# Optimization experiments

Measured on AMD Instinct MI355X. Metric: run time of the kernel, lower is better.

The kernel has to match this reference:

```python
import jax, jax.numpy as jnp
import numpy as np

B, N, C_IN, C_OUT, M = 32, 4096, 128, 128, 256


def setup_inputs() -> dict:
    key = jax.random.key(0)
    k1, k2, k3, k4 = jax.random.split(key, 4)
    x = jax.random.normal(k1, (B, N, C_IN), dtype=jnp.float32)
    # Lowest-M eigenvectors of a graph Laplacian are orthonormal columns [N, M];
    # build an equivalent orthonormal basis via QR of a random matrix.
    U, _ = jnp.linalg.qr(jax.random.normal(k2, (N, M), dtype=jnp.float32))
    # complex spectral weights ~ 0.02 * randn (cfloat) split into real/imag parts
    W_real = jax.random.normal(k3, (C_IN, C_OUT, M), dtype=jnp.float32) * 0.02
    W_imag = jax.random.normal(k4, (C_IN, C_OUT, M), dtype=jnp.float32) * 0.02
    return {"x": x, "eigenvectors": U, "W_real": W_real, "W_imag": W_imag}


def reference(x, eigenvectors, W_real, W_imag):
    # Graph Fourier transform: project node features onto spectral modes.
    # x_spec[b, m, c] = sum_n U[n, m] * x[b, n, c]
    x_spec = jnp.einsum('nm,bnc->bmc', eigenvectors, x)  # [B, M, C_in], real
    # Per-mode complex channel mixing, fused into one batched einsum.
    # Original takes .real of (x_spec * W); since x_spec is real,
    # Re(x_spec @ W) = x_spec @ Re(W), so W_imag does not affect the output.
    out_spec_real = jnp.einsum('bmc,com->bmo', x_spec, W_real)  # [B, M, C_out]
    # Inverse graph Fourier transform back to node space.
    return jnp.einsum('nm,bmo->bno', eigenvectors, out_spec_real)  # [B, N, C_out]
```

## Files before the change

kernel.cpp:

```cpp
#include <hip/hip_runtime.h>
#include <hip/hip_bf16.h>

#define BB 32
#define NN 4096
#define CI 128
#define CO 128
#define MM 256
#define KS 8

typedef __hip_bfloat16 bf16;
typedef __attribute__((ext_vector_type(8))) short bf16x8;
typedef __attribute__((ext_vector_type(4))) float f32x4;

__device__ inline void gl_lds16(const void* g, void* l) {
    __builtin_amdgcn_global_load_lds(
        (const __attribute__((address_space(1))) void*)g,
        (__attribute__((address_space(3))) void*)l, 16, 0, 0);
}

__global__ __launch_bounds__(256) void k_cvtU(const float* __restrict__ U,
                                              bf16* __restrict__ Un,
                                              bf16* __restrict__ Ut) {
    const int n0 = blockIdx.x * 64;
    const int m0 = blockIdx.y * 64;
    __shared__ float tile[64][65];
    const int t = threadIdx.x;
    #pragma unroll
    for (int i = 0; i < 16; ++i) {
        int lin = t + i * 256;
        int r = lin >> 6, c = lin & 63;
        float v = U[(n0 + r) * MM + m0 + c];
        tile[r][c] = v;
        Un[(n0 + r) * MM + m0 + c] = __float2bfloat16(v);
    }
    __syncthreads();
    #pragma unroll
    for (int pass = 0; pass < 2; ++pass) {
        int no = t & 7;
        int m  = (t >> 3) + pass * 32;
        bf16 tmp[8];
        #pragma unroll
        for (int j = 0; j < 8; ++j) tmp[j] = __float2bfloat16(tile[no * 8 + j][m]);
        *(bf16x8*)&Ut[(long)(m0 + m) * NN + n0 + no * 8] = *(bf16x8*)tmp;
    }
}

__global__ __launch_bounds__(256) void k_wt(const float* __restrict__ W,
                                            bf16* __restrict__ Wt) {
    const int m0 = blockIdx.x * 64;
    const int o0 = blockIdx.y * 64;
    const int c  = blockIdx.z;
    __shared__ float tile[64][65];
    const int t = threadIdx.x;
    #pragma unroll
    for (int pass = 0; pass < 4; ++pass) {
        int r  = (t >> 4) + pass * 16;
        int m4 = (t & 15) * 4;
        float4 v = *(const float4*)&W[((long)c * CO + o0 + r) * MM + m0 + m4];
        tile[r][m4 + 0] = v.x; tile[r][m4 + 1] = v.y;
        tile[r][m4 + 2] = v.z; tile[r][m4 + 3] = v.w;
    }
    __syncthreads();
    #pragma unroll
    for (int pass = 0; pass < 2; ++pass) {
        int oo = t & 7;
        int m  = (t >> 3) + pass * 32;
        bf16 tmp[8];
        #pragma unroll
        for (int j = 0; j < 8; ++j) tmp[j] = __float2bfloat16(tile[oo * 8 + j][m]);
        *(bf16x8*)&Wt[((long)(m0 + m) * CI + c) * CO + o0 + oo * 8] = *(bf16x8*)tmp;
    }
}

__global__ __launch_bounds__(512) void k_gemm1f(const bf16* __restrict__ Ut,
                                                const float* __restrict__ x,
                                                bf16* __restrict__ part) {
    const int ks = blockIdx.x;
    const int b  = blockIdx.y;
    __shared__ __align__(16) bf16  As[2][MM * 32];
    __shared__ __align__(16) bf16  Bs[2][CI * 32];
    __shared__ __align__(16) float Xf[2][32 * CI];
    const int t    = threadIdx.x;
    const int lane = t & 63;
    const int wave = t >> 6;
    const int wm   = wave >> 1, wn = wave & 1;
    const int fr   = lane & 15;
    const int kg   = (lane >> 4) * 8;
    f32x4 acc[4][4] = {};
    const long xrow  = (long)b * NN;
    const int  kbase = ks * 512;

    auto STAGE = [&](int buf, int kt) {
        const int k0 = kbase + kt * 32;
        #pragma unroll
        for (int i = 0; i < 2; ++i) {
            int lin = t + i * 512;
            {
                int r = lin >> 2, kk = (lin & 3) * 8;
                gl_lds16(&Ut[(long)r * NN + k0 + kk], &As[buf][lin * 8]);
            }
            {
                int r = lin >> 5, c4 = (lin & 31) * 4;
                gl_lds16(&x[(xrow + k0 + r) * CI + c4], &Xf[buf][lin * 4]);
            }
        }
    };

    const int NT = 512 / 32;
    STAGE(0, 0);
    __syncthreads();
    #pragma unroll
    for (int kt = 0; kt < NT; ++kt) {
        const int cur = kt & 1;
        if (kt + 1 < NT) STAGE(cur ^ 1, kt + 1);
        {
            const int c  = t & 127;
            const int nh = t >> 7;
            bf16 tmp[8];
            #pragma unroll
            for (int j = 0; j < 8; ++j)
                tmp[j] = __float2bfloat16(Xf[cur][(nh * 8 + j) * CI + c]);
            *(bf16x8*)&Bs[cur][c * 32 + nh * 8] = *(bf16x8*)tmp;
        }
        __syncthreads();
        bf16x8 a[4], bfr[4];
        #pragma unroll
        for (int i = 0; i < 4; ++i)
            a[i] = *(const bf16x8*)&As[cur][(wm * 64 + i * 16 + fr) * 32 + kg];
        #pragma unroll
        for (int j = 0; j < 4; ++j)
            bfr[j] = *(const bf16x8*)&Bs[cur][(wn * 64 + j * 16 + fr) * 32 + kg];
        #pragma unroll
        for (int i = 0; i < 4; ++i)
            #pragma unroll
            for (int j = 0; j < 4; ++j)
                acc[i][j] = __builtin_amdgcn_mfma_f32_16x16x32_bf16(a[i], bfr[j], acc[i][j], 0, 0, 0);
        __syncthreads();
    }
    const int quad = (lane >> 4) * 4;
    const long pbase = ((long)ks * BB + b) * MM * CI;
    #pragma unroll
    for (int i = 0; i < 4; ++i) {
        #pragma unroll
        for (int j = 0; j < 4; ++j) {
            int mg = wm * 64 + i * 16 + quad;
            int cg = wn * 64 + j * 16 + fr;
            #pragma unroll
            for (int r = 0; r < 4; ++r)
                part[pbase + (long)(mg + r) * CI + cg] = __float2bfloat16(acc[i][j][r]);
        }
    }
}

__global__ __launch_bounds__(256) void k_mix(const bf16* __restrict__ part,
                                             const bf16* __restrict__ Wt,
                                             bf16* __restrict__ osT) {
    const int blk = blockIdx.x;
    const int m   = (blk & 7) * 32 + (blk >> 3);
    __shared__ bf16  Wl[CI][CO];
    __shared__ float xl[CI][36];
    const int t = threadIdx.x;
    const long wb = (long)m * CI * CO;
    #pragma unroll
    for (int i = 0; i < 8; ++i) {
        int ch = t + i * 256;
        int c = ch >> 4, og = (ch & 15) * 8;
        *(bf16x8*)&Wl[c][og] = *(const bf16x8*)&Wt[wb + (long)c * CO + og];
    }
    #pragma unroll
    for (int i = 0; i < 2; ++i) {
        int ch = t + i * 256;
        int b = ch >> 4, c8 = (ch & 15) * 8;
        float s[8] = {};
        #pragma unroll
        for (int ks = 0; ks < KS; ++ks) {
            bf16x8 v = *(const bf16x8*)&part[(((long)ks * BB + b) * MM + m) * CI + c8];
            #pragma unroll
            for (int j = 0; j < 8; ++j) s[j] += __bfloat162float(((const bf16*)&v)[j]);
        }
        #pragma unroll
        for (int j = 0; j < 8; ++j) xl[c8 + j][b] = s[j];
    }
    __syncthreads();
    const int o  = t & 127;
    const int bh = t >> 7;
    float acc[16] = {};
    for (int c = 0; c < CI; ++c) {
        float w = __bfloat162float(Wl[c][o]);
        #pragma unroll
        for (int j = 0; j < 16; ++j)
            acc[j] += xl[c][bh * 16 + j] * w;
    }
    #pragma unroll
    for (int j = 0; j < 16; ++j)
        osT[((long)(bh * 16 + j) * CO + o) * MM + m] = __float2bfloat16(acc[j]);
}

__global__ __launch_bounds__(256) void k_gemm3(const bf16* __restrict__ Un,
                                               const bf16* __restrict__ osT,
                                               float* __restrict__ out) {
    const int n0 = blockIdx.x * 128;
    const int b  = blockIdx.y;
    __shared__ __align__(16) bf16 As[128 * 32];
    __shared__ __align__(16) bf16 Bs[128 * 32];
    const int t    = threadIdx.x;
    const int lane = t & 63;
    const int wave = t >> 6;
    const int wm   = wave >> 1, wn = wave & 1;
    const int fr   = lane & 15;
    const int kg   = (lane >> 4) * 8;
    f32x4 acc[4][4] = {};
    const long bbase = (long)b * CO * MM;
    for (int kt = 0; kt < MM / 32; ++kt) {
        const int k0 = kt * 32;
        #pragma unroll
        for (int i = 0; i < 2; ++i) {
            int lin = t + i * 256;
            int r = lin >> 2, kk = (lin & 3) * 8;
            gl_lds16(&Un[(long)(n0 + r) * MM + k0 + kk], &As[lin * 8]);
            gl_lds16(&osT[bbase + (long)r * MM + k0 + kk], &Bs[lin * 8]);
        }
        __syncthreads();
        bf16x8 a[4], bfr[4];
        #pragma unroll
        for (int i = 0; i < 4; ++i)
            a[i] = *(const bf16x8*)&As[(wm * 64 + i * 16 + fr) * 32 + kg];
        #pragma unroll
        for (int j = 0; j < 4; ++j)
            bfr[j] = *(const bf16x8*)&Bs[(wn * 64 + j * 16 + fr) * 32 + kg];
        #pragma unroll
        for (int i = 0; i < 4; ++i)
            #pragma unroll
            for (int j = 0; j < 4; ++j)
                acc[i][j] = __builtin_amdgcn_mfma_f32_16x16x32_bf16(a[i], bfr[j], acc[i][j], 0, 0, 0);
        __syncthreads();
    }
    const int quad = (lane >> 4) * 4;
    #pragma unroll
    for (int i = 0; i < 4; ++i) {
        #pragma unroll
        for (int j = 0; j < 4; ++j) {
            int ng = n0 + wm * 64 + i * 16 + quad;
            int og = wn * 64 + j * 16 + fr;
            #pragma unroll
            for (int r = 0; r < 4; ++r)
                out[((long)b * NN + ng + r) * CO + og] = acc[i][j][r];
        }
    }
}

extern "C" void kernel_launch(void* const* d_in, const int* in_sizes, int n_in,
                              void* d_out, int out_size, void* d_ws, size_t ws_size,
                              hipStream_t stream) {
    const float* x  = (const float*)d_in[0];
    const float* U  = (const float*)d_in[1];
    const float* Wr = (const float*)d_in[2];
    float* out = (float*)d_out;

    char* p = (char*)d_ws;
    bf16* part = (bf16*)p;  p += (size_t)KS * BB * MM * CI * 2;
    bf16* Ut   = (bf16*)p;  p += (size_t)MM * NN * 2;
    bf16* Un   = (bf16*)p;  p += (size_t)NN * MM * 2;
    bf16* osT  = (bf16*)p;  p += (size_t)BB * CO * MM * 2;
    bf16* Wt   = (bf16*)p;  p += (size_t)MM * CI * CO * 2;

    k_cvtU  <<<dim3(NN / 64, MM / 64), 256, 0, stream>>>(U, Un, Ut);
    k_wt    <<<dim3(MM / 64, CO / 64, CI), 256, 0, stream>>>(Wr, Wt);
    k_gemm1f<<<dim3(KS, BB), 512, 0, stream>>>(Ut, x, part);
    k_mix   <<<dim3(256), 256, 0, stream>>>(part, Wt, osT);
    k_gemm3 <<<dim3(NN / 128, BB), 256, 0, stream>>>(Un, osT, out);
}
```

Baseline: 187.7 us.

## Double-buffer gemm3 LDS loads with explicit vmcnt waits and reorder gemm1 prefetch

```diff
diff --git a/kernel.cpp b/kernel.cpp
--- a/kernel.cpp
+++ b/kernel.cpp
@@ -17,6 +17,9 @@
         (const __attribute__((address_space(1))) void*)g,
         (__attribute__((address_space(3))) void*)l, 16, 0, 0);
 }
+
+#define CFENCE() asm volatile("" ::: "memory")
+#define BAR()    __builtin_amdgcn_s_barrier()
 
 __global__ __launch_bounds__(256) void k_cvtU(const float* __restrict__ U,
                                               bf16* __restrict__ Un,
@@ -112,7 +115,6 @@
     #pragma unroll
     for (int kt = 0; kt < NT; ++kt) {
         const int cur = kt & 1;
-        if (kt + 1 < NT) STAGE(cur ^ 1, kt + 1);
         {
             const int c  = t & 127;
             const int nh = t >> 7;
@@ -123,6 +125,7 @@
             *(bf16x8*)&Bs[cur][c * 32 + nh * 8] = *(bf16x8*)tmp;
         }
         __syncthreads();
+        if (kt + 1 < NT) STAGE(cur ^ 1, kt + 1);
         bf16x8 a[4], bfr[4];
         #pragma unroll
         for (int i = 0; i < 4; ++i)
@@ -201,8 +204,8 @@
                                                float* __restrict__ out) {
     const int n0 = blockIdx.x * 128;
     const int b  = blockIdx.y;
-    __shared__ __align__(16) bf16 As[128 * 32];
-    __shared__ __align__(16) bf16 Bs[128 * 32];
+    __shared__ __align__(16) bf16 As[2][128 * 32];
+    __shared__ __align__(16) bf16 Bs[2][128 * 32];
     const int t    = threadIdx.x;
     const int lane = t & 63;
     const int wave = t >> 6;
@@ -211,29 +214,43 @@
     const int kg   = (lane >> 4) * 8;
     f32x4 acc[4][4] = {};
     const long bbase = (long)b * CO * MM;
-    for (int kt = 0; kt < MM / 32; ++kt) {
+
+    auto STAGE = [&](int buf, int kt) {
         const int k0 = kt * 32;
         #pragma unroll
         for (int i = 0; i < 2; ++i) {
             int lin = t + i * 256;
             int r = lin >> 2, kk = (lin & 3) * 8;
-            gl_lds16(&Un[(long)(n0 + r) * MM + k0 + kk], &As[lin * 8]);
-            gl_lds16(&osT[bbase + (long)r * MM + k0 + kk], &Bs[lin * 8]);
-        }
-        __syncthreads();
+            gl_lds16(&Un[(long)(n0 + r) * MM + k0 + kk], &As[buf][lin * 8]);
+            gl_lds16(&osT[bbase + (long)r * MM + k0 + kk], &Bs[buf][lin * 8]);
+        }
+    };
+
+    const int NT = MM / 32;
+    STAGE(0, 0);
+    #pragma unroll
+    for (int kt = 0; kt < NT; ++kt) {
+        const int cur = kt & 1;
+        if (kt + 1 < NT) {
+            STAGE(cur ^ 1, kt + 1);
+            asm volatile("s_waitcnt vmcnt(4)" ::: "memory");
+        } else {
+            asm volatile("s_waitcnt vmcnt(0)" ::: "memory");
+        }
+        BAR(); CFENCE();
         bf16x8 a[4], bfr[4];
         #pragma unroll
         for (int i = 0; i < 4; ++i)
-            a[i] = *(const bf16x8*)&As[(wm * 64 + i * 16 + fr) * 32 + kg];
+            a[i] = *(const bf16x8*)&As[cur][(wm * 64 + i * 16 + fr) * 32 + kg];
         #pragma unroll
         for (int j = 0; j < 4; ++j)
-            bfr[j] = *(const bf16x8*)&Bs[(wn * 64 + j * 16 + fr) * 32 + kg];
+            bfr[j] = *(const bf16x8*)&Bs[cur][(wn * 64 + j * 16 + fr) * 32 + kg];
         #pragma unroll
         for (int i = 0; i < 4; ++i)
             #pragma unroll
             for (int j = 0; j < 4; ++j)
                 acc[i][j] = __builtin_amdgcn_mfma_f32_16x16x32_bf16(a[i], bfr[j], acc[i][j], 0, 0, 0);
-        __syncthreads();
+        CFENCE(); BAR(); CFENCE();
     }
     const int quad = (lane >> 4) * 4;
     #pragma unroll
```

After: 187.5 us. Within noise of the previous version (-0.1%).

## Fuse all five stages into one cooperative persistent kernel with grid syncs

Applied to the files above, without the earlier changes.

```diff
diff --git a/kernel.cpp b/kernel.cpp
--- a/kernel.cpp
+++ b/kernel.cpp
@@ -1,5 +1,8 @@
 #include <hip/hip_runtime.h>
 #include <hip/hip_bf16.h>
+#include <hip/hip_cooperative_groups.h>
+
+namespace cg = cooperative_groups;
 
 #define BB 32
 #define NN 4096
@@ -16,6 +19,251 @@
     __builtin_amdgcn_global_load_lds(
         (const __attribute__((address_space(1))) void*)g,
         (__attribute__((address_space(3))) void*)l, 16, 0, 0);
+}
+
+__global__ __launch_bounds__(256, 2) void k_all(const float* __restrict__ x,
+                                                const float* __restrict__ U,
+                                                const float* __restrict__ W,
+                                                float* __restrict__ out,
+                                                bf16* __restrict__ part,
+                                                bf16* __restrict__ Ut,
+                                                bf16* __restrict__ Un,
+                                                bf16* __restrict__ osT,
+                                                bf16* __restrict__ Wt) {
+    cg::grid_group grid = cg::this_grid();
+    const int blk = blockIdx.x;
+    const int t   = threadIdx.x;
+    __shared__ __align__(16) char smem[64 * 1024];
+
+    if (blk < 256) {
+        const int n0 = (blk & 63) * 64;
+        const int m0 = (blk >> 6) * 64;
+        float (*tile)[65] = (float(*)[65])smem;
+        #pragma unroll
+        for (int i = 0; i < 16; ++i) {
+            int lin = t + i * 256;
+            int r = lin >> 6, c = lin & 63;
+            float v = U[(n0 + r) * MM + m0 + c];
+            tile[r][c] = v;
+            Un[(n0 + r) * MM + m0 + c] = __float2bfloat16(v);
+        }
+        __syncthreads();
+        #pragma unroll
+        for (int pass = 0; pass < 2; ++pass) {
+            int no = t & 7;
+            int m  = (t >> 3) + pass * 32;
+            bf16 tmp[8];
+            #pragma unroll
+            for (int j = 0; j < 8; ++j) tmp[j] = __float2bfloat16(tile[no * 8 + j][m]);
+            *(bf16x8*)&Ut[(long)(m0 + m) * NN + n0 + no * 8] = *(bf16x8*)tmp;
+        }
+    } else {
+        const int q  = blk - 256;
+        const int m0 = (q & 3) * 64;
+        const int o0 = ((q >> 2) & 1) * 64;
+        const int cb = q >> 3;
+        float (*tile)[65] = (float(*)[65])smem;
+        for (int ci = 0; ci < 4; ++ci) {
+            const int c = cb * 4 + ci;
+            #pragma unroll
+            for (int pass = 0; pass < 4; ++pass) {
+                int r  = (t >> 4) + pass * 16;
+                int m4 = (t & 15) * 4;
+                float4 v = *(const float4*)&W[((long)c * CO + o0 + r) * MM + m0 + m4];
+                tile[r][m4 + 0] = v.x; tile[r][m4 + 1] = v.y;
+                tile[r][m4 + 2] = v.z; tile[r][m4 + 3] = v.w;
+            }
+            __syncthreads();
+            #pragma unroll
+            for (int pass = 0; pass < 2; ++pass) {
+                int oo = t & 7;
+                int m  = (t >> 3) + pass * 32;
+                bf16 tmp[8];
+                #pragma unroll
+                for (int j = 0; j < 8; ++j) tmp[j] = __float2bfloat16(tile[oo * 8 + j][m]);
+                *(bf16x8*)&Wt[((long)(m0 + m) * CI + c) * CO + o0 + oo * 8] = *(bf16x8*)tmp;
+            }
+            __syncthreads();
+        }
+    }
+    __threadfence();
+    grid.sync();
+
+    {
+        const int ks = blk & 7;
+        const int mt = (blk >> 3) & 1;
+        const int b  = blk >> 4;
+        const int m0 = mt * 128;
+        bf16*  As = (bf16*)smem;
+        bf16*  Bs = (bf16*)(smem + 16 * 1024);
+        float* Xf = (float*)(smem + 32 * 1024);
+        const int lane = t & 63, wave = t >> 6;
+        const int wm = wave >> 1, wn = wave & 1;
+        const int fr = lane & 15, kg = (lane >> 4) * 8;
+        f32x4 acc[4][4] = {};
+        const long xrow  = (long)b * NN;
+        const int  kbase = ks * 512;
+
+        auto STAGE1 = [&](int buf, int kt) {
+            const int k0 = kbase + kt * 32;
+            #pragma unroll
+            for (int i = 0; i < 2; ++i) {
+                int lin = t + i * 256;
+                int r = lin >> 2, kk = (lin & 3) * 8;
+                gl_lds16(&Ut[(long)(m0 + r) * NN + k0 + kk], &As[buf * 4096 + lin * 8]);
+            }
+            #pragma unroll
+            for (int i = 0; i < 4; ++i) {
+                int lin = t + i * 256;
+                int r = lin >> 5, c4 = (lin & 31) * 4;
+                gl_lds16(&x[(xrow + k0 + r) * CI + c4], &Xf[buf * 4096 + lin * 4]);
+            }
+        };
+
+        STAGE1(0, 0);
+        __syncthreads();
+        for (int kt = 0; kt < 16; ++kt) {
+            const int cur = kt & 1;
+            {
+                const int c = t & 127;
+                #pragma unroll
+                for (int pass = 0; pass < 2; ++pass) {
+                    int no = (t >> 7) + pass * 2;
+                    bf16 tmp[8];
+                    #pragma unroll
+                    for (int j = 0; j < 8; ++j)
+                        tmp[j] = __float2bfloat16(Xf[cur * 4096 + (no * 8 + j) * CI + c]);
+                    *(bf16x8*)&Bs[cur * 4096 + c * 32 + no * 8] = *(bf16x8*)tmp;
+                }
+            }
+            __syncthreads();
+            if (kt + 1 < 16) STAGE1(cur ^ 1, kt + 1);
+            bf16x8 a[4], bfr[4];
+            #pragma unroll
+            for (int i = 0; i < 4; ++i)
+                a[i] = *(const bf16x8*)&As[cur * 4096 + (wm * 64 + i * 16 + fr) * 32 + kg];
+            #pragma unroll
+            for (int j = 0; j < 4; ++j)
+                bfr[j] = *(const bf16x8*)&Bs[cur * 4096 + (wn * 64 + j * 16 + fr) * 32 + kg];
+            #pragma unroll
+            for (int i = 0; i < 4; ++i)
+                #pragma unroll
+                for (int j = 0; j < 4; ++j)
+                    acc[i][j] = __builtin_amdgcn_mfma_f32_16x16x32_bf16(a[i], bfr[j], acc[i][j], 0, 0, 0);
+            __syncthreads();
+        }
+        const int quad = (lane >> 4) * 4;
+        const long pbase = ((long)ks * BB + b) * MM * CI;
+        #pragma unroll
+        for (int i = 0; i < 4; ++i) {
+            #pragma unroll
+            for (int j = 0; j < 4; ++j) {
+                int mg = m0 + wm * 64 + i * 16 + quad;
+                int cg = wn * 64 + j * 16 + fr;
+                #pragma unroll
+                for (int r = 0; r < 4; ++r)
+                    part[pbase + (long)(mg + r) * CI + cg] = __float2bfloat16(acc[i][j][r]);
+            }
+        }
+    }
+    __threadfence();
+    grid.sync();
+
+    {
+        const int mi = blk >> 1;
+        const int m  = (mi & 7) * 32 + (mi >> 3);
+        const int o0 = (blk & 1) * 64;
+        float* Wl = (float*)smem;
+        float* xl = (float*)(smem + 32 * 1024);
+        const long wb = (long)m * CI * CO;
+        #pragma unroll
+        for (int i = 0; i < 4; ++i) {
+            int ch = t + i * 256;
+            int c = ch >> 3, og = (ch & 7) * 8;
+            bf16x8 v = *(const bf16x8*)&Wt[wb + (long)c * CO + o0 + og];
+            #pragma unroll
+            for (int j = 0; j < 8; ++j) Wl[c * 64 + og + j] = __bfloat162float(((const bf16*)&v)[j]);
+        }
+        #pragma unroll
+        for (int i = 0; i < 2; ++i) {
+            int ch = t + i * 256;
+            int b2 = ch >> 4, c8 = (ch & 15) * 8;
+            float s[8] = {};
+            #pragma unroll
+            for (int ks = 0; ks < KS; ++ks) {
+                bf16x8 v = *(const bf16x8*)&part[(((long)ks * BB + b2) * MM + m) * CI + c8];
+                #pragma unroll
+                for (int j = 0; j < 8; ++j) s[j] += __bfloat162float(((const bf16*)&v)[j]);
+            }
+            #pragma unroll
+            for (int j = 0; j < 8; ++j) xl[(c8 + j) * 36 + b2] = s[j];
+        }
+        __syncthreads();
+        const int op = t & 63;
+        const int bq = t >> 6;
+        float acc[8] = {};
+        for (int c = 0; c < CI; ++c) {
+            float w = Wl[c * 64 + op];
+            #pragma unroll
+            for (int j = 0; j < 8; ++j)
+                acc[j] += xl[c * 36 + bq * 8 + j] * w;
+        }
+        #pragma unroll
+        for (int j = 0; j < 8; ++j)
+            osT[((long)(bq * 8 + j) * CO + o0 + op) * MM + m] = __float2bfloat16(acc[j]);
+    }
+    __threadfence();
+    grid.sync();
+
+    {
+        const int b3 = blk >> 4;
+        bf16* As3 = (bf16*)smem;
+        bf16* Bs3 = (bf16*)(smem + 8 * 1024);
+        const int lane = t & 63, wave = t >> 6;
+        const int wm = wave >> 1, wn = wave & 1;
+        const int fr = lane & 15, kg = (lane >> 4) * 8;
+        const long bbase = (long)b3 * CO * MM;
+        for (int rr = 0; rr < 2; ++rr) {
+            const int n0 = ((blk & 15) * 2 + rr) * 128;
+            f32x4 acc[4][4] = {};
+            for (int kt = 0; kt < MM / 32; ++kt) {
+                const int k0 = kt * 32;
+                #pragma unroll
+                for (int i = 0; i < 2; ++i) {
+                    int lin = t + i * 256;
+                    int r = lin >> 2, kk = (lin & 3) * 8;
+                    gl_lds16(&Un[(long)(n0 + r) * MM + k0 + kk], &As3[lin * 8]);
+                    gl_lds16(&osT[bbase + (long)r * MM + k0 + kk], &Bs3[lin * 8]);
+                }
+                __syncthreads();
+                bf16x8 a[4], bfr[4];
+                #pragma unroll
+                for (int i = 0; i < 4; ++i)
+                    a[i] = *(const bf16x8*)&As3[(wm * 64 + i * 16 + fr) * 32 + kg];
+                #pragma unroll
+                for (int j = 0; j < 4; ++j)
+                    bfr[j] = *(const bf16x8*)&Bs3[(wn * 64 + j * 16 + fr) * 32 + kg];
+                #pragma unroll
+                for (int i = 0; i < 4; ++i)
+                    #pragma unroll
+                    for (int j = 0; j < 4; ++j)
+                        acc[i][j] = __builtin_amdgcn_mfma_f32_16x16x32_bf16(a[i], bfr[j], acc[i][j], 0, 0, 0);
+                __syncthreads();
+            }
+            const int quad = (lane >> 4) * 4;
+            #pragma unroll
+            for (int i = 0; i < 4; ++i) {
+                #pragma unroll
+                for (int j = 0; j < 4; ++j) {
+                    int ng = n0 + wm * 64 + i * 16 + quad;
+                    int og = wn * 64 + j * 16 + fr;
+                    #pragma unroll
+                    for (int r = 0; r < 4; ++r)
+                        out[((long)b3 * NN + ng + r) * CO + og] = acc[i][j][r];
+                }
+            }
+        }
+    }
 }
 
 __global__ __launch_bounds__(256) void k_cvtU(const float* __restrict__ U,
@@ -112,7 +360,6 @@
     #pragma unroll
     for (int kt = 0; kt < NT; ++kt) {
         const int cur = kt & 1;
-        if (kt + 1 < NT) STAGE(cur ^ 1, kt + 1);
         {
             const int c  = t & 127;
             const int nh = t >> 7;
@@ -123,6 +370,7 @@
             *(bf16x8*)&Bs[cur][c * 32 + nh * 8] = *(bf16x8*)tmp;
         }
         __syncthreads();
+        if (kt + 1 < NT) STAGE(cur ^ 1, kt + 1);
         bf16x8 a[4], bfr[4];
         #pragma unroll
         for (int i = 0; i < 4; ++i)
@@ -264,9 +512,19 @@
     bf16* osT  = (bf16*)p;  p += (size_t)BB * CO * MM * 2;
     bf16* Wt   = (bf16*)p;  p += (size_t)MM * CI * CO * 2;
 
-    k_cvtU  <<<dim3(NN / 64, MM / 64), 256, 0, stream>>>(U, Un, Ut);
-    k_wt    <<<dim3(MM / 64, CO / 64, CI), 256, 0, stream>>>(Wr, Wt);
-    k_gemm1f<<<dim3(KS, BB), 512, 0, stream>>>(Ut, x, part);
-    k_mix   <<<dim3(256), 256, 0, stream>>>(part, Wt, osT);
-    k_gemm3 <<<dim3(NN / 128, BB), 256, 0, stream>>>(Un, osT, out);
-}
+    const float* xa = x; const float* Ua = U; const float* Wa = Wr;
+    float* outa = out;
+    bf16 *parta = part, *Uta = Ut, *Una = Un, *osTa = osT, *Wta = Wt;
+    void* args[] = {&xa, &Ua, &Wa, &outa, &parta, &Uta, &Una, &osTa, &Wta};
+
+    hipError_t err = hipLaunchCooperativeKernel((const void*)k_all,
+                                                dim3(512), dim3(256),
+                                                args, 0, stream);
+    if (err != hipSuccess) {
+        k_cvtU  <<<dim3(NN / 64, MM / 64), 256, 0, stream>>>(U, Un, Ut);
+        k_wt    <<<dim3(MM / 64, CO / 64, CI), 256, 0, stream>>>(Wr, Wt);
+        k_gemm1f<<<dim3(KS, BB), 512, 0, stream>>>(Ut, x, part);
+        k_mix   <<<dim3(256), 256, 0, stream>>>(part, Wt, osT);
+        k_gemm3 <<<dim3(NN / 128, BB), 256, 0, stream>>>(Un, osT, out);
+    }
+}
```

Result: slower. 579.0 us (+208.4%).

## Merge prep kernels into one launch and split GEMM1 into 128-row M tiles

Applied to the files above, without the earlier changes.

```diff
diff --git a/kernel.cpp b/kernel.cpp
--- a/kernel.cpp
+++ b/kernel.cpp
@@ -18,68 +18,72 @@
         (__attribute__((address_space(3))) void*)l, 16, 0, 0);
 }
 
-__global__ __launch_bounds__(256) void k_cvtU(const float* __restrict__ U,
+__global__ __launch_bounds__(256) void k_prep(const float* __restrict__ U,
+                                              const float* __restrict__ W,
                                               bf16* __restrict__ Un,
-                                              bf16* __restrict__ Ut) {
-    const int n0 = blockIdx.x * 64;
-    const int m0 = blockIdx.y * 64;
+                                              bf16* __restrict__ Ut,
+                                              bf16* __restrict__ Wt) {
+    const int blk = blockIdx.x;
+    const int t = threadIdx.x;
     __shared__ float tile[64][65];
-    const int t = threadIdx.x;
-    #pragma unroll
-    for (int i = 0; i < 16; ++i) {
-        int lin = t + i * 256;
-        int r = lin >> 6, c = lin & 63;
-        float v = U[(n0 + r) * MM + m0 + c];
-        tile[r][c] = v;
-        Un[(n0 + r) * MM + m0 + c] = __float2bfloat16(v);
-    }
-    __syncthreads();
-    #pragma unroll
-    for (int pass = 0; pass < 2; ++pass) {
-        int no = t & 7;
-        int m  = (t >> 3) + pass * 32;
-        bf16 tmp[8];
-        #pragma unroll
-        for (int j = 0; j < 8; ++j) tmp[j] = __float2bfloat16(tile[no * 8 + j][m]);
-        *(bf16x8*)&Ut[(long)(m0 + m) * NN + n0 + no * 8] = *(bf16x8*)tmp;
-    }
-}
-
-__global__ __launch_bounds__(256) void k_wt(const float* __restrict__ W,
-                                            bf16* __restrict__ Wt) {
-    const int m0 = blockIdx.x * 64;
-    const int o0 = blockIdx.y * 64;
-    const int c  = blockIdx.z;
-    __shared__ float tile[64][65];
-    const int t = threadIdx.x;
-    #pragma unroll
-    for (int pass = 0; pass < 4; ++pass) {
-        int r  = (t >> 4) + pass * 16;
-        int m4 = (t & 15) * 4;
-        float4 v = *(const float4*)&W[((long)c * CO + o0 + r) * MM + m0 + m4];
-        tile[r][m4 + 0] = v.x; tile[r][m4 + 1] = v.y;
-        tile[r][m4 + 2] = v.z; tile[r][m4 + 3] = v.w;
-    }
-    __syncthreads();
-    #pragma unroll
-    for (int pass = 0; pass < 2; ++pass) {
-        int oo = t & 7;
-        int m  = (t >> 3) + pass * 32;
-        bf16 tmp[8];
-        #pragma unroll
-        for (int j = 0; j < 8; ++j) tmp[j] = __float2bfloat16(tile[oo * 8 + j][m]);
-        *(bf16x8*)&Wt[((long)(m0 + m) * CI + c) * CO + o0 + oo * 8] = *(bf16x8*)tmp;
-    }
-}
-
-__global__ __launch_bounds__(512) void k_gemm1f(const bf16* __restrict__ Ut,
+    if (blk < 256) {
+        const int n0 = (blk & 63) * 64;
+        const int m0 = (blk >> 6) * 64;
+        #pragma unroll
+        for (int i = 0; i < 16; ++i) {
+            int lin = t + i * 256;
+            int r = lin >> 6, c = lin & 63;
+            float v = U[(n0 + r) * MM + m0 + c];
+            tile[r][c] = v;
+            Un[(n0 + r) * MM + m0 + c] = __float2bfloat16(v);
+        }
+        __syncthreads();
+        #pragma unroll
+        for (int pass = 0; pass < 2; ++pass) {
+            int no = t & 7;
+            int m  = (t >> 3) + pass * 32;
+            bf16 tmp[8];
+            #pragma unroll
+            for (int j = 0; j < 8; ++j) tmp[j] = __float2bfloat16(tile[no * 8 + j][m]);
+            *(bf16x8*)&Ut[(long)(m0 + m) * NN + n0 + no * 8] = *(bf16x8*)tmp;
+        }
+    } else {
+        const int q  = blk - 256;
+        const int c  = q >> 3;
+        const int m0 = (q & 3) * 64;
+        const int o0 = ((q >> 2) & 1) * 64;
+        #pragma unroll
+        for (int pass = 0; pass < 4; ++pass) {
+            int r  = (t >> 4) + pass * 16;
+            int m4 = (t & 15) * 4;
+            float4 v = *(const float4*)&W[((long)c * CO + o0 + r) * MM + m0 + m4];
+            tile[r][m4 + 0] = v.x; tile[r][m4 + 1] = v.y;
+            tile[r][m4 + 2] = v.z; tile[r][m4 + 3] = v.w;
+        }
+        __syncthreads();
+        #pragma unroll
+        for (int pass = 0; pass < 2; ++pass) {
+            int oo = t & 7;
+            int m  = (t >> 3) + pass * 32;
+            bf16 tmp[8];
+            #pragma unroll
+            for (int j = 0; j < 8; ++j) tmp[j] = __float2bfloat16(tile[oo * 8 + j][m]);
+            *(bf16x8*)&Wt[((long)(m0 + m) * CI + c) * CO + o0 + oo * 8] = *(bf16x8*)tmp;
+        }
+    }
+}
+
+__global__ __launch_bounds__(256) void k_gemm1f(const bf16* __restrict__ Ut,
                                                 const float* __restrict__ x,
                                                 bf16* __restrict__ part) {
-    const int ks = blockIdx.x;
-    const int b  = blockIdx.y;
-    __shared__ __align__(16) bf16  As[2][MM * 32];
-    __shared__ __align__(16) bf16  Bs[2][CI * 32];
-    __shared__ __align__(16) float Xf[2][32 * CI];
+    const int bx = blockIdx.x;
+    const int ks = bx & 7;
+    const int mt = (bx >> 3) & 1;
+    const int b  = bx >> 4;
+    const int m0 = mt * 128;
+    __shared__ __align__(16) bf16  As[2][128 * 32];
+    __shared__ __align__(16) bf16  Bs[2][128 * 32];
+    __shared__ __align__(16) float Xf[2][32 * 128];
     const int t    = threadIdx.x;
     const int lane = t & 63;
     const int wave = t >> 6;
@@ -94,35 +98,36 @@
         const int k0 = kbase + kt * 32;
         #pragma unroll
         for (int i = 0; i < 2; ++i) {
-            int lin = t + i * 512;
-            {
-                int r = lin >> 2, kk = (lin & 3) * 8;
-                gl_lds16(&Ut[(long)r * NN + k0 + kk], &As[buf][lin * 8]);
-            }
-            {
-                int r = lin >> 5, c4 = (lin & 31) * 4;
-                gl_lds16(&x[(xrow + k0 + r) * CI + c4], &Xf[buf][lin * 4]);
-            }
+            int lin = t + i * 256;
+            int r = lin >> 2, kk = (lin & 3) * 8;
+            gl_lds16(&Ut[(long)(m0 + r) * NN + k0 + kk], &As[buf][lin * 8]);
+        }
+        #pragma unroll
+        for (int i = 0; i < 4; ++i) {
+            int lin = t + i * 256;
+            int r = lin >> 5, c4 = (lin & 31) * 4;
+            gl_lds16(&x[(xrow + k0 + r) * CI + c4], &Xf[buf][lin * 4]);
         }
     };
 
-    const int NT = 512 / 32;
     STAGE(0, 0);
     __syncthreads();
-    #pragma unroll
-    for (int kt = 0; kt < NT; ++kt) {
+    for (int kt = 0; kt < 16; ++kt) {
         const int cur = kt & 1;
-        if (kt + 1 < NT) STAGE(cur ^ 1, kt + 1);
         {
-            const int c  = t & 127;
-            const int nh = t >> 7;
-            bf16 tmp[8];
-            #pragma unroll
-            for (int j = 0; j < 8; ++j)
-                tmp[j] = __float2bfloat16(Xf[cur][(nh * 8 + j) * CI + c]);
-            *(bf16x8*)&Bs[cur][c * 32 + nh * 8] = *(bf16x8*)tmp;
-        }
-        __syncthreads();
+            const int c = t & 127;
+            #pragma unroll
+            for (int pass = 0; pass < 2; ++pass) {
+                int no = (t >> 7) + pass * 2;
+                bf16 tmp[8];
+                #pragma unroll
+                for (int j = 0; j < 8; ++j)
+                    tmp[j] = __float2bfloat16(Xf[cur][(no * 8 + j) * 128 + c]);
+                *(bf16x8*)&Bs[cur][c * 32 + no * 8] = *(bf16x8*)tmp;
+            }
+        }
+        __syncthreads();
+        if (kt + 1 < 16) STAGE(cur ^ 1, kt + 1);
         bf16x8 a[4], bfr[4];
         #pragma unroll
         for (int i = 0; i < 4; ++i)
@@ -143,7 +148,7 @@
     for (int i = 0; i < 4; ++i) {
         #pragma unroll
         for (int j = 0; j < 4; ++j) {
-            int mg = wm * 64 + i * 16 + quad;
+            int mg = m0 + wm * 64 + i * 16 + quad;
             int cg = wn * 64 + j * 16 + fr;
             #pragma unroll
             for (int r = 0; r < 4; ++r)
@@ -264,9 +269,8 @@
     bf16* osT  = (bf16*)p;  p += (size_t)BB * CO * MM * 2;
     bf16* Wt   = (bf16*)p;  p += (size_t)MM * CI * CO * 2;
 
-    k_cvtU  <<<dim3(NN / 64, MM / 64), 256, 0, stream>>>(U, Un, Ut);
-    k_wt    <<<dim3(MM / 64, CO / 64, CI), 256, 0, stream>>>(Wr, Wt);
-    k_gemm1f<<<dim3(KS, BB), 512, 0, stream>>>(Ut, x, part);
+    k_prep  <<<dim3(1280), 256, 0, stream>>>(U, Wr, Un, Ut, Wt);
+    k_gemm1f<<<dim3(KS * 2 * BB), 256, 0, stream>>>(Ut, x, part);
     k_mix   <<<dim3(256), 256, 0, stream>>>(part, Wt, osT);
     k_gemm3 <<<dim3(NN / 128, BB), 256, 0, stream>>>(Un, osT, out);
 }
```

After: 182.9 us. 1.03x faster.
